# Kernel tuning notes

Hardware: AMD Instinct MI355X
Metric: run time of the kernel (lower is better)

The kernel has to match this reference:

```python
import jax, jax.numpy as jnp
import numpy as np

EPS = 1e-05


def layer_norm(x, a, b):
    m = jnp.mean(x, axis=-1, keepdims=True)
    v = jnp.var(x, axis=-1, keepdims=True)
    return a * (x - m) / jnp.sqrt(v + EPS) + b


def setup_inputs() -> dict:
    key = jax.random.key(0)
    ks = jax.random.split(key, 16)
    b, n, d, h = 1, 384, 128, 128
    s = 1.0 / np.sqrt(d)
    inp = {
        "x": jax.random.normal(ks[0], (b, n, n, d), dtype=jnp.float32),
        "norm_a": jnp.ones((d,), jnp.float32),
        "norm_b": jnp.zeros((d,), jnp.float32),
        "Wl": jax.random.normal(ks[1], (d, h), jnp.float32) * s,
        "bl": jnp.zeros((h,), jnp.float32),
        "Wr": jax.random.normal(ks[2], (d, h), jnp.float32) * s,
        "br": jnp.zeros((h,), jnp.float32),
        "Wlg": jax.random.normal(ks[3], (d, h), jnp.float32) * s,
        "blg": jnp.ones((h,), jnp.float32),
        "Wrg": jax.random.normal(ks[4], (d, h), jnp.float32) * s,
        "brg": jnp.ones((h,), jnp.float32),
        "Wog": jax.random.normal(ks[5], (d, h), jnp.float32) * s,
        "bog": jnp.ones((h,), jnp.float32),
        "on_a": jnp.ones((h,), jnp.float32),
        "on_b": jnp.zeros((h,), jnp.float32),
        "Wo": jax.random.normal(ks[6], (h, d), jnp.float32) * s,
        "bo": jnp.zeros((d,), jnp.float32),
    }
    return inp


def reference(x, norm_a, norm_b, Wl, bl, Wr, br, Wlg, blg, Wrg, brg, Wog, bog, on_a, on_b, Wo, bo):
    n = x.shape[1]
    xn = layer_norm(x, norm_a, norm_b)
    left = (xn @ Wl + bl) * jax.nn.sigmoid(xn @ Wlg + blg)
    right = (xn @ Wr + br) * jax.nn.sigmoid(xn @ Wrg + brg)
    out_gate = jax.nn.sigmoid(xn @ Wog + bog)
    # ingoing mix: out[b,i,j,d] = sum_k left[b,k,j,d] * right[b,k,i,d], in fp32
    out = jnp.einsum('bkjd,bkid->bijd', left.astype(jnp.float32), right.astype(jnp.float32)) / n
    out = out.astype(x.dtype)
    out = layer_norm(out, on_a, on_b) * out_gate
    return out @ Wo + bo
```

## Files before the change

### kernel.cpp

```cpp
#include <hip/hip_runtime.h>
#include <hip/hip_bf16.h>

#define NN 384
#define DD 128
#define MM (NN*NN)

typedef __attribute__((ext_vector_type(8))) short short8;
typedef __attribute__((ext_vector_type(4))) float f32x4;

__device__ __forceinline__ unsigned short f2bf(float f){
  unsigned u = __float_as_uint(f);
  u += 0x7fffu + ((u >> 16) & 1u);
  return (unsigned short)(u >> 16);
}
__device__ __forceinline__ float bf2f(unsigned short u){
  return __uint_as_float(((unsigned)u) << 16);
}
__device__ __forceinline__ float sigm(float x){
  return 1.0f / (1.0f + __expf(-x));
}
__device__ __forceinline__ unsigned cvtpk(float lo, float hi){
  unsigned r;
  asm("v_cvt_pk_bf16_f32 %0, %1, %2" : "=v"(r) : "v"(lo), "v"(hi));
  return r;
}
__device__ __forceinline__ f32x4 mfma16(short8 a, short8 b, f32x4 c){
  return __builtin_amdgcn_mfma_f32_16x16x32_bf16(a, b, c, 0, 0, 0);
}
__device__ __forceinline__ void gll16(const void* g, void* l){
  __builtin_amdgcn_global_load_lds(
      (const __attribute__((address_space(1))) unsigned int*)g,
      (__attribute__((address_space(3))) unsigned int*)l, 16, 0, 0);
}

__global__ void k_prep(const float* __restrict__ Wl, const float* __restrict__ Wlg,
                       const float* __restrict__ Wr, const float* __restrict__ Wrg,
                       const float* __restrict__ Wog, const float* __restrict__ Wo,
                       unsigned short* __restrict__ Wcat, unsigned short* __restrict__ Wot){
  int n = blockIdx.x;
  if(n < 640){
    const float* src; int col;
    if(n < 128){ src = Wl;  col = n; }
    else if(n < 256){ src = Wlg; col = n-128; }
    else if(n < 384){ src = Wr;  col = n-256; }
    else if(n < 512){ src = Wrg; col = n-384; }
    else            { src = Wog; col = n-512; }
    for(int k = threadIdx.x; k < 128; k += 64)
      Wcat[n*128 + k] = f2bf(src[k*128 + col]);
  } else {
    int c = n - 640;
    for(int k = threadIdx.x; k < 128; k += 64)
      Wot[c*128 + k] = f2bf(Wo[k*128 + c]);
  }
}

__global__ __launch_bounds__(256) void k_ln_x(const float* __restrict__ x,
    const float* __restrict__ na, const float* __restrict__ nb,
    unsigned short* __restrict__ xn){
  int wid = threadIdx.x >> 6, lane = threadIdx.x & 63;
  long r = (long)blockIdx.x*4 + wid;
  float2 v = *(const float2*)(x + r*DD + lane*2);
  float s  = v.x + v.y;
  float sq = v.x*v.x + v.y*v.y;
  #pragma unroll
  for(int m = 32; m >= 1; m >>= 1){ s += __shfl_xor(s, m); sq += __shfl_xor(sq, m); }
  float mean = s  * (1.0f/128.0f);
  float var  = sq * (1.0f/128.0f) - mean*mean;
  float rstd = rsqrtf(var + 1e-5f);
  float2 a = *(const float2*)(na + lane*2);
  float2 b = *(const float2*)(nb + lane*2);
  unsigned pk = (unsigned)f2bf(a.x*(v.x-mean)*rstd + b.x)
              | ((unsigned)f2bf(a.y*(v.y-mean)*rstd + b.y) << 16);
  *(unsigned*)(xn + r*DD + lane*2) = pk;
}

__global__ __launch_bounds__(512, 4) void k_proj(
    const unsigned short* __restrict__ xn, const unsigned short* __restrict__ Wcat,
    const float* __restrict__ bl, const float* __restrict__ blg,
    const float* __restrict__ br, const float* __restrict__ brg,
    const float* __restrict__ bog,
    unsigned short* __restrict__ Lt, unsigned short* __restrict__ Rt,
    unsigned short* __restrict__ gate){
  __shared__ char lds[65536];
  const int tid = threadIdx.x;
  const int wid = tid >> 6, lane = tid & 63;
  const int lrow = lane & 15, lgrp = lane >> 4;
  const int b = blockIdx.x;
  const int xcd = b & 7, slot = b >> 3;

  if(slot < 576){
    const int t = (slot >> 2)*8 + xcd;
    const int f = slot & 3;
    const int j0 = (t / 6)*2, k0 = (t % 6)*64;

    {
      int rsub = lane >> 4, c = lane & 15;
      #pragma unroll
      for(int p = 0; p < 4; ++p){
        int r0 = wid*16 + p*4;
        int r = r0 + rsub;
        long gr = (long)(k0 + (r & 63))*NN + (j0 + (r >> 6));
        gll16(xn + gr*DD + (c ^ (r & 7))*8, &lds[r0*256]);
      }
      #pragma unroll
      for(int p = 0; p < 4; ++p){
        int n0 = wid*16 + p*4;
        int nl = n0 + rsub;
        int ng = (nl >> 5)*128 + f*32 + (nl & 31);
        gll16(Wcat + ng*DD + (c ^ (nl & 7))*8, &lds[32768 + n0*256]);
      }
    }
    __syncthreads();

    const int ws = wid >> 2;
    const int wd = (wid >> 1) & 1;
    const int wr = wid & 1;
    f32x4 zero = {0.f,0.f,0.f,0.f};
    f32x4 acc[4][2];
    #pragma unroll
    for(int a1=0;a1<4;++a1){ acc[a1][0] = zero; acc[a1][1] = zero; }

    #pragma unroll 2
    for(int ks = 0; ks < 4; ++ks){
      int nlv = ws*64 + wd*16 + lrow;
      short8 bv = *(const short8*)(&lds[32768 + nlv*256 + (((ks*4+lgrp)*16) ^ ((nlv&7)<<4))]);
      int nlg = nlv + 32;
      short8 bg = *(const short8*)(&lds[32768 + nlg*256 + (((ks*4+lgrp)*16) ^ ((nlg&7)<<4))]);
      #pragma unroll
      for(int fr = 0; fr < 4; ++fr){
        int r = wr*64 + fr*16 + lrow;
        short8 af = *(const short8*)(&lds[r*256 + (((ks*4+lgrp)*16) ^ ((r&7)<<4))]);
        acc[fr][0] = mfma16(af, bv, acc[fr][0]);
        acc[fr][1] = mfma16(af, bg, acc[fr][1]);
      }
    }

    const int d = f*32 + wd*16 + lrow;
    const float b0v = (ws ? br  : bl )[d];
    const float b1v = (ws ? brg : blg)[d];
    const float sc = ws ? 1.0f : (1.0f/384.0f);
    unsigned short* dst = (ws ? Rt : Lt) + (long)d*MM + (long)(j0 + wr)*NN + k0;
    #pragma unroll
    for(int fr = 0; fr < 4; ++fr){
      float v0 = (acc[fr][0][0] + b0v)*sigm(acc[fr][1][0] + b1v)*sc;
      float v1 = (acc[fr][0][1] + b0v)*sigm(acc[fr][1][1] + b1v)*sc;
      float v2 = (acc[fr][0][2] + b0v)*sigm(acc[fr][1][2] + b1v)*sc;
      float v3 = (acc[fr][0][3] + b0v)*sigm(acc[fr][1][3] + b1v)*sc;
      uint2 pk; pk.x = cvtpk(v0, v1); pk.y = cvtpk(v2, v3);
      *(uint2*)(dst + fr*16 + lgrp*4) = pk;
    }
  } else {
    const int m = (slot - 576)*8 + xcd;
    {
      int rsub = lane >> 4, c = lane & 15;
      #pragma unroll
      for(int p = 0; p < 4; ++p){
        int r0 = wid*16 + p*4;
        int r = r0 + rsub;
        long gr = (long)m*128 + r;
        gll16(xn + gr*DD + (c ^ (r & 7))*8, &lds[r0*256]);
      }
      #pragma unroll
      for(int p = 0; p < 4; ++p){
        int n0 = wid*16 + p*4;
        int nl = n0 + rsub;
        gll16(Wcat + (512 + nl)*DD + (c ^ (nl & 7))*8, &lds[32768 + n0*256]);
      }
    }
    __syncthreads();

    const int wm = wid >> 2;
    const int wc = wid & 3;
    f32x4 zero = {0.f,0.f,0.f,0.f};
    f32x4 acc[2][4];
    #pragma unroll
    for(int a1=0;a1<2;++a1)
      #pragma unroll
      for(int a2=0;a2<4;++a2) acc[a1][a2] = zero;

    #pragma unroll 2
    for(int ks = 0; ks < 4; ++ks){
      short8 af[2];
      #pragma unroll
      for(int cf = 0; cf < 2; ++cf){
        int nl = wc*32 + cf*16 + lrow;
        af[cf] = *(const short8*)(&lds[32768 + nl*256 + (((ks*4+lgrp)*16) ^ ((nl&7)<<4))]);
      }
      #pragma unroll
      for(int mf = 0; mf < 4; ++mf){
        int r = wm*64 + mf*16 + lrow;
        short8 bfr = *(const short8*)(&lds[r*256 + (((ks*4+lgrp)*16) ^ ((r&7)<<4))]);
        acc[0][mf] = mfma16(af[0], bfr, acc[0][mf]);
        acc[1][mf] = mfma16(af[1], bfr, acc[1][mf]);
      }
    }

    #pragma unroll
    for(int cf = 0; cf < 2; ++cf){
      int c = wc*32 + cf*16 + lgrp*4;
      float4 bo4 = *(const float4*)(bog + c);
      #pragma unroll
      for(int mf = 0; mf < 4; ++mf){
        int rr = wm*64 + mf*16 + lrow;
        float v0 = sigm(acc[cf][mf][0] + bo4.x);
        float v1 = sigm(acc[cf][mf][1] + bo4.y);
        float v2 = sigm(acc[cf][mf][2] + bo4.z);
        float v3 = sigm(acc[cf][mf][3] + bo4.w);
        uint2 pk; pk.x = cvtpk(v0, v1); pk.y = cvtpk(v2, v3);
        *(uint2*)(gate + ((long)m*128 + rr)*DD + c) = pk;
      }
    }
  }
}

__global__ __launch_bounds__(256) void k_einsum(
    const unsigned short* __restrict__ Rt, const unsigned short* __restrict__ Lt,
    unsigned short* __restrict__ mid){
  __shared__ char lds[65536];
  const int b = blockIdx.x;
  const int xcd = b & 7, slot = b >> 3;
  const int d = (slot/9)*8 + xcd;
  const int t = slot % 9;
  const int it = t/3, jt = t%3;
  const int i0 = it*128, j0 = jt*128;
  const unsigned short* Abase = Lt + (long)d*MM;
  const unsigned short* Bbase = Rt + (long)d*MM;
  const int wid = threadIdx.x >> 6, lane = threadIdx.x & 63;
  const int wr = wid >> 1, wc = wid & 1;
  const int lrow = lane & 15, lgrp = lane >> 4;

  auto stage = [&](int buf, int kt){
    int k = kt*64;
    int c = lane & 7;
    #pragma unroll
    for(int t8 = 0; t8 < 8; ++t8){
      int rr = wid*64 + t8*8 + (lane >> 3);
      int r = rr & 127;
      const unsigned short* src = (rr < 128) ? (Abase + (long)(j0+r)*NN + k)
                                             : (Bbase + (long)(i0+r)*NN + k);
      gll16(src + (c ^ (r & 7))*8, &lds[buf*32768 + (wid*64 + t8*8)*128]);
    }
  };

  f32x4 zero = {0.f,0.f,0.f,0.f};
  f32x4 acc[4][4];
  #pragma unroll
  for(int a1 = 0; a1 < 4; ++a1)
    #pragma unroll
    for(int a2 = 0; a2 < 4; ++a2) acc[a1][a2] = zero;

  stage(0, 0);
  __syncthreads();
  for(int kt = 0; kt < 6; ++kt){
    int cur = kt & 1;
    if(kt < 5) stage(cur ^ 1, kt + 1);
    const int base = cur*32768;
    #pragma unroll
    for(int ks = 0; ks < 2; ++ks){
      short8 af[4], bf[4];
      #pragma unroll
      for(int f = 0; f < 4; ++f){
        int rj = wr*64 + f*16 + lrow;
        af[f] = *(const short8*)(&lds[base + rj*128 + (((ks*4+lgrp)*16) ^ ((rj & 7) << 4))]);
        int ri = wc*64 + f*16 + lrow;
        bf[f] = *(const short8*)(&lds[base + 16384 + ri*128 + (((ks*4+lgrp)*16) ^ ((ri & 7) << 4))]);
      }
      #pragma unroll
      for(int fj = 0; fj < 4; ++fj)
        #pragma unroll
        for(int fi = 0; fi < 4; ++fi)
          acc[fj][fi] = mfma16(af[fj], bf[fi], acc[fj][fi]);
    }
    __syncthreads();
  }

  #pragma unroll
  for(int fj = 0; fj < 4; ++fj){
    int j = j0 + wr*64 + fj*16 + lgrp*4;
    #pragma unroll
    for(int fi = 0; fi < 4; ++fi){
      int i = i0 + wc*64 + fi*16 + lrow;
      uint2 pk;
      pk.x = cvtpk(acc[fj][fi][0], acc[fj][fi][1]);
      pk.y = cvtpk(acc[fj][fi][2], acc[fj][fi][3]);
      *(uint2*)(mid + (long)d*MM + (long)i*NN + j) = pk;
    }
  }
}

__global__ __launch_bounds__(256) void k_final(
    const unsigned short* __restrict__ mid, const unsigned short* __restrict__ gate,
    const float* __restrict__ ona, const float* __restrict__ onb,
    const unsigned short* __restrict__ Wot, const float* __restrict__ bo,
    float* __restrict__ out){
  __shared__ float midt[64][129];
  __shared__ char vlds[16384];
  const int tid = threadIdx.x;
  const int i = blockIdx.y;
  const int j0 = blockIdx.x*64;

  {
    int jp = tid & 15, dr = tid >> 4;
    #pragma unroll
    for(int pass = 0; pass < 8; ++pass){
      int dd = pass*16 + dr;
      uint2 v = *(const uint2*)(mid + (long)dd*MM + (long)i*NN + j0 + jp*4);
      midt[jp*4+0][dd] = bf2f((unsigned short)(v.x & 0xffffu));
      midt[jp*4+1][dd] = bf2f((unsigned short)(v.x >> 16));
      midt[jp*4+2][dd] = bf2f((unsigned short)(v.y & 0xffffu));
      midt[jp*4+3][dd] = bf2f((unsigned short)(v.y >> 16));
    }
  }
  __syncthreads();

  {
    int j = tid >> 2, s = tid & 3;
    float sum = 0.f, sq = 0.f;
    #pragma unroll
    for(int o = 0; o < 32; ++o){ float v = midt[j][s*32 + o]; sum += v; sq += v*v; }
    #pragma unroll
    for(int m = 1; m < 4; m <<= 1){ sum += __shfl_xor(sum, m); sq += __shfl_xor(sq, m); }
    float mean = sum*(1.f/128.f);
    float var  = sq *(1.f/128.f) - mean*mean;
    float rstd = rsqrtf(var + 1e-5f);
    long gr = ((long)i*NN + j0 + j)*DD;
    #pragma unroll
    for(int o = 0; o < 32; o += 4){
      int dd = s*32 + o;
      uint2 gv = *(const uint2*)(gate + gr + dd);
      float g0 = bf2f((unsigned short)(gv.x & 0xffffu));
      float g1 = bf2f((unsigned short)(gv.x >> 16));
      float g2 = bf2f((unsigned short)(gv.y & 0xffffu));
      float g3 = bf2f((unsigned short)(gv.y >> 16));
      float v0 = (ona[dd]  *(midt[j][dd]  -mean)*rstd + onb[dd]  )*g0;
      float v1 = (ona[dd+1]*(midt[j][dd+1]-mean)*rstd + onb[dd+1])*g1;
      float v2 = (ona[dd+2]*(midt[j][dd+2]-mean)*rstd + onb[dd+2])*g2;
      float v3 = (ona[dd+3]*(midt[j][dd+3]-mean)*rstd + onb[dd+3])*g3;
      unsigned pk01 = cvtpk(v0, v1);
      unsigned pk23 = cvtpk(v2, v3);
      *(unsigned*)(&vlds[j*256 + ((dd*2)     ^ ((j & 7) << 4))]) = pk01;
      *(unsigned*)(&vlds[j*256 + ((dd*2 + 4) ^ ((j & 7) << 4))]) = pk23;
    }
  }
  __syncthreads();

  const int wid = tid >> 6, lane = tid & 63;
  const int lrow = lane & 15, lgrp = lane >> 4;
  f32x4 zero = {0.f,0.f,0.f,0.f};
  f32x4 acc[8];
  #pragma unroll
  for(int fc = 0; fc < 8; ++fc) acc[fc] = zero;
  #pragma unroll 1
  for(int ks = 0; ks < 4; ++ks){
    int row = wid*16 + lrow;
    short8 a = *(const short8*)(&vlds[row*256 + (((ks*4+lgrp)*16) ^ ((row & 7) << 4))]);
    #pragma unroll
    for(int fc = 0; fc < 8; ++fc){
      int n = fc*16 + lrow;
      short8 bfr = *(const short8*)(Wot + n*128 + ks*32 + lgrp*8);
      acc[fc] = mfma16(a, bfr, acc[fc]);
    }
  }
  #pragma unroll
  for(int fc = 0; fc < 8; ++fc){
    int c = fc*16 + lrow;
    float bb = bo[c];
    #pragma unroll
    for(int q = 0; q < 4; ++q){
      int jl = wid*16 + lgrp*4 + q;
      out[((long)i*NN + j0 + jl)*DD + c] = acc[fc][q] + bb;
    }
  }
}

extern "C" void kernel_launch(void* const* d_in, const int* in_sizes, int n_in,
                              void* d_out, int out_size, void* d_ws, size_t ws_size,
                              hipStream_t stream){
  const float* x   = (const float*)d_in[0];
  const float* na  = (const float*)d_in[1];
  const float* nb  = (const float*)d_in[2];
  const float* Wl  = (const float*)d_in[3];
  const float* bl  = (const float*)d_in[4];
  const float* Wr  = (const float*)d_in[5];
  const float* br  = (const float*)d_in[6];
  const float* Wlg = (const float*)d_in[7];
  const float* blg = (const float*)d_in[8];
  const float* Wrg = (const float*)d_in[9];
  const float* brg = (const float*)d_in[10];
  const float* Wog = (const float*)d_in[11];
  const float* bog = (const float*)d_in[12];
  const float* ona = (const float*)d_in[13];
  const float* onb = (const float*)d_in[14];
  const float* Wo  = (const float*)d_in[15];
  const float* bo  = (const float*)d_in[16];
  float* out = (float*)d_out;

  char* ws = (char*)d_ws;
  const size_t SZ = (size_t)MM*DD*2;
  unsigned short* xn   = (unsigned short*)(ws);
  unsigned short* Lt   = (unsigned short*)(ws + SZ);
  unsigned short* Rt   = (unsigned short*)(ws + 2*SZ);
  unsigned short* gate = (unsigned short*)(ws + 3*SZ);
  unsigned short* Wcat = (unsigned short*)(ws + 4*SZ);
  unsigned short* Wot  = (unsigned short*)(ws + 4*SZ + (size_t)640*128*2);
  unsigned short* mid  = xn;

  k_prep  <<<768, 64, 0, stream>>>(Wl, Wlg, Wr, Wrg, Wog, Wo, Wcat, Wot);
  k_ln_x  <<<MM/4, 256, 0, stream>>>(x, na, nb, xn);
  k_proj  <<<5760, 512, 0, stream>>>(xn, Wcat, bl, blg, br, brg, bog, Lt, Rt, gate);
  k_einsum<<<1152, 256, 0, stream>>>(Rt, Lt, mid);
  k_final <<<dim3(6, 384), 256, 0, stream>>>(mid, gate, ona, onb, Wot, bo, out);
}
```

Measured before the change: 200.3 us.

## Move output-gate projection into final kernel and make proj kernel persistent with double buffering

New measurement: 197.2 us. Within noise of the previous version (-1.6%).

```diff
diff --git a/kernel.cpp b/kernel.cpp
--- a/kernel.cpp
+++ b/kernel.cpp
@@ -74,72 +74,70 @@
   *(unsigned*)(xn + r*DD + lane*2) = pk;
 }
 
-__global__ __launch_bounds__(512, 4) void k_proj(
+__global__ __launch_bounds__(256, 4) void k_proj(
     const unsigned short* __restrict__ xn, const unsigned short* __restrict__ Wcat,
     const float* __restrict__ bl, const float* __restrict__ blg,
     const float* __restrict__ br, const float* __restrict__ brg,
-    const float* __restrict__ bog,
-    unsigned short* __restrict__ Lt, unsigned short* __restrict__ Rt,
-    unsigned short* __restrict__ gate){
-  __shared__ char lds[65536];
+    unsigned short* __restrict__ Lt, unsigned short* __restrict__ Rt){
+  __shared__ char lds[2][16384];
   const int tid = threadIdx.x;
   const int wid = tid >> 6, lane = tid & 63;
   const int lrow = lane & 15, lgrp = lane >> 4;
   const int b = blockIdx.x;
-  const int xcd = b & 7, slot = b >> 3;
-
-  if(slot < 576){
-    const int t = (slot >> 2)*8 + xcd;
-    const int f = slot & 3;
-    const int j0 = (t / 6)*2, k0 = (t % 6)*64;
-
-    {
-      int rsub = lane >> 4, c = lane & 15;
-      #pragma unroll
-      for(int p = 0; p < 4; ++p){
-        int r0 = wid*16 + p*4;
-        int r = r0 + rsub;
-        long gr = (long)(k0 + (r & 63))*NN + (j0 + (r >> 6));
-        gll16(xn + gr*DD + (c ^ (r & 7))*8, &lds[r0*256]);
-      }
-      #pragma unroll
-      for(int p = 0; p < 4; ++p){
-        int n0 = wid*16 + p*4;
-        int nl = n0 + rsub;
-        int ng = (nl >> 5)*128 + f*32 + (nl & 31);
-        gll16(Wcat + ng*DD + (c ^ (nl & 7))*8, &lds[32768 + n0*256]);
-      }
-    }
-    __syncthreads();
-
-    const int ws = wid >> 2;
-    const int wd = (wid >> 1) & 1;
-    const int wr = wid & 1;
+  const int f = b / 288;
+  const int w = b % 288;
+
+  const int ws = wid >> 1;
+  const int wd = wid & 1;
+  const int d  = f*32 + wd*16 + lrow;
+
+  short8 bv[4], bg[4];
+  #pragma unroll
+  for(int ks = 0; ks < 4; ++ks){
+    bv[ks] = *(const short8*)(Wcat + (ws*256 + d)*DD + ks*32 + lgrp*8);
+    bg[ks] = *(const short8*)(Wcat + (ws*256 + 128 + d)*DD + ks*32 + lgrp*8);
+  }
+  const float b0v = (ws ? br  : bl )[d];
+  const float b1v = (ws ? brg : blg)[d];
+  const float sc  = ws ? 1.0f : (1.0f/384.0f);
+  unsigned short* const base = (ws ? Rt : Lt) + (long)d*MM;
+
+  auto stage = [&](int buf, int v){
+    int j = v/6, kb = v%6;
+    int rsub = lane >> 4, c = lane & 15;
+    #pragma unroll
+    for(int p = 0; p < 4; ++p){
+      int r0 = p*16 + wid*4;
+      int r = r0 + rsub;
+      gll16(xn + ((long)(kb*64 + r)*NN + j)*DD + (c ^ (r & 7))*8, &lds[buf][r0*256]);
+    }
+  };
+
+  stage(0, w*8);
+  __syncthreads();
+  int cur = 0;
+  for(int i = 0; i < 8; ++i){
+    int v = w*8 + i;
+    if(i < 7) stage(cur^1, v+1);
+
     f32x4 zero = {0.f,0.f,0.f,0.f};
     f32x4 acc[4][2];
     #pragma unroll
     for(int a1=0;a1<4;++a1){ acc[a1][0] = zero; acc[a1][1] = zero; }
 
-    #pragma unroll 2
+    #pragma unroll
     for(int ks = 0; ks < 4; ++ks){
-      int nlv = ws*64 + wd*16 + lrow;
-      short8 bv = *(const short8*)(&lds[32768 + nlv*256 + (((ks*4+lgrp)*16) ^ ((nlv&7)<<4))]);
-      int nlg = nlv + 32;
-      short8 bg = *(const short8*)(&lds[32768 + nlg*256 + (((ks*4+lgrp)*16) ^ ((nlg&7)<<4))]);
       #pragma unroll
       for(int fr = 0; fr < 4; ++fr){
-        int r = wr*64 + fr*16 + lrow;
-        short8 af = *(const short8*)(&lds[r*256 + (((ks*4+lgrp)*16) ^ ((r&7)<<4))]);
-        acc[fr][0] = mfma16(af, bv, acc[fr][0]);
-        acc[fr][1] = mfma16(af, bg, acc[fr][1]);
-      }
-    }
-
-    const int d = f*32 + wd*16 + lrow;
-    const float b0v = (ws ? br  : bl )[d];
-    const float b1v = (ws ? brg : blg)[d];
-    const float sc = ws ? 1.0f : (1.0f/384.0f);
-    unsigned short* dst = (ws ? Rt : Lt) + (long)d*MM + (long)(j0 + wr)*NN + k0;
+        int r = fr*16 + lrow;
+        short8 af = *(const short8*)(&lds[cur][r*256 + (((ks*4+lgrp)*16) ^ ((r&7)<<4))]);
+        acc[fr][0] = mfma16(af, bv[ks], acc[fr][0]);
+        acc[fr][1] = mfma16(af, bg[ks], acc[fr][1]);
+      }
+    }
+
+    int j = v/6, kb = v%6;
+    unsigned short* dst = base + (long)j*NN + kb*64;
     #pragma unroll
     for(int fr = 0; fr < 4; ++fr){
       float v0 = (acc[fr][0][0] + b0v)*sigm(acc[fr][1][0] + b1v)*sc;
@@ -149,67 +147,8 @@
       uint2 pk; pk.x = cvtpk(v0, v1); pk.y = cvtpk(v2, v3);
       *(uint2*)(dst + fr*16 + lgrp*4) = pk;
     }
-  } else {
-    const int m = (slot - 576)*8 + xcd;
-    {
-      int rsub = lane >> 4, c = lane & 15;
-      #pragma unroll
-      for(int p = 0; p < 4; ++p){
-        int r0 = wid*16 + p*4;
-        int r = r0 + rsub;
-        long gr = (long)m*128 + r;
-        gll16(xn + gr*DD + (c ^ (r & 7))*8, &lds[r0*256]);
-      }
-      #pragma unroll
-      for(int p = 0; p < 4; ++p){
-        int n0 = wid*16 + p*4;
-        int nl = n0 + rsub;
-        gll16(Wcat + (512 + nl)*DD + (c ^ (nl & 7))*8, &lds[32768 + n0*256]);
-      }
-    }
     __syncthreads();
-
-    const int wm = wid >> 2;
-    const int wc = wid & 3;
-    f32x4 zero = {0.f,0.f,0.f,0.f};
-    f32x4 acc[2][4];
-    #pragma unroll
-    for(int a1=0;a1<2;++a1)
-      #pragma unroll
-      for(int a2=0;a2<4;++a2) acc[a1][a2] = zero;
-
-    #pragma unroll 2
-    for(int ks = 0; ks < 4; ++ks){
-      short8 af[2];
-      #pragma unroll
-      for(int cf = 0; cf < 2; ++cf){
-        int nl = wc*32 + cf*16 + lrow;
-        af[cf] = *(const short8*)(&lds[32768 + nl*256 + (((ks*4+lgrp)*16) ^ ((nl&7)<<4))]);
-      }
-      #pragma unroll
-      for(int mf = 0; mf < 4; ++mf){
-        int r = wm*64 + mf*16 + lrow;
-        short8 bfr = *(const short8*)(&lds[r*256 + (((ks*4+lgrp)*16) ^ ((r&7)<<4))]);
-        acc[0][mf] = mfma16(af[0], bfr, acc[0][mf]);
-        acc[1][mf] = mfma16(af[1], bfr, acc[1][mf]);
-      }
-    }
-
-    #pragma unroll
-    for(int cf = 0; cf < 2; ++cf){
-      int c = wc*32 + cf*16 + lgrp*4;
-      float4 bo4 = *(const float4*)(bog + c);
-      #pragma unroll
-      for(int mf = 0; mf < 4; ++mf){
-        int rr = wm*64 + mf*16 + lrow;
-        float v0 = sigm(acc[cf][mf][0] + bo4.x);
-        float v1 = sigm(acc[cf][mf][1] + bo4.y);
-        float v2 = sigm(acc[cf][mf][2] + bo4.z);
-        float v3 = sigm(acc[cf][mf][3] + bo4.w);
-        uint2 pk; pk.x = cvtpk(v0, v1); pk.y = cvtpk(v2, v3);
-        *(uint2*)(gate + ((long)m*128 + rr)*DD + c) = pk;
-      }
-    }
+    cur ^= 1;
   }
 }
 
@@ -289,15 +228,37 @@
 }
 
 __global__ __launch_bounds__(256) void k_final(
-    const unsigned short* __restrict__ mid, const unsigned short* __restrict__ gate,
+    const unsigned short* __restrict__ mid, const unsigned short* __restrict__ xn,
+    const unsigned short* __restrict__ Wcat,
+    const float* __restrict__ bog,
     const float* __restrict__ ona, const float* __restrict__ onb,
     const unsigned short* __restrict__ Wot, const float* __restrict__ bo,
     float* __restrict__ out){
-  __shared__ float midt[64][129];
-  __shared__ char vlds[16384];
+  __shared__ unsigned short midt[64][144];
+  __shared__ char slds[16384];
+  __shared__ char glds[16384];
   const int tid = threadIdx.x;
+  const int wid = tid >> 6, lane = tid & 63;
+  const int lrow = lane & 15, lgrp = lane >> 4;
   const int i = blockIdx.y;
   const int j0 = blockIdx.x*64;
+
+  {
+    int rsub = lane >> 4, c = lane & 15;
+    #pragma unroll
+    for(int p = 0; p < 4; ++p){
+      int r0 = p*16 + wid*4;
+      int r = r0 + rsub;
+      gll16(xn + ((long)i*NN + j0 + r)*DD + (c ^ (r & 7))*8, &slds[r0*256]);
+    }
+  }
+  const int wc = wid;
+  short8 ag[2][4];
+  #pragma unroll
+  for(int cf = 0; cf < 2; ++cf)
+    #pragma unroll
+    for(int ks = 0; ks < 4; ++ks)
+      ag[cf][ks] = *(const short8*)(Wcat + (512 + wc*32 + cf*16 + lrow)*DD + ks*32 + lgrp*8);
 
   {
     int jp = tid & 15, dr = tid >> 4;
@@ -305,70 +266,114 @@
     for(int pass = 0; pass < 8; ++pass){
       int dd = pass*16 + dr;
       uint2 v = *(const uint2*)(mid + (long)dd*MM + (long)i*NN + j0 + jp*4);
-      midt[jp*4+0][dd] = bf2f((unsigned short)(v.x & 0xffffu));
-      midt[jp*4+1][dd] = bf2f((unsigned short)(v.x >> 16));
-      midt[jp*4+2][dd] = bf2f((unsigned short)(v.y & 0xffffu));
-      midt[jp*4+3][dd] = bf2f((unsigned short)(v.y >> 16));
+      midt[jp*4+0][dd] = (unsigned short)(v.x & 0xffffu);
+      midt[jp*4+1][dd] = (unsigned short)(v.x >> 16);
+      midt[jp*4+2][dd] = (unsigned short)(v.y & 0xffffu);
+      midt[jp*4+3][dd] = (unsigned short)(v.y >> 16);
+    }
+  }
+  __syncthreads();
+
+  {
+    f32x4 zero = {0.f,0.f,0.f,0.f};
+    f32x4 accg[2][4];
+    #pragma unroll
+    for(int a1=0;a1<2;++a1)
+      #pragma unroll
+      for(int a2=0;a2<4;++a2) accg[a1][a2] = zero;
+    #pragma unroll
+    for(int ks = 0; ks < 4; ++ks){
+      short8 bx[4];
+      #pragma unroll
+      for(int mf = 0; mf < 4; ++mf){
+        int r = mf*16 + lrow;
+        bx[mf] = *(const short8*)(&slds[r*256 + (((ks*4+lgrp)*16) ^ ((r&7)<<4))]);
+      }
+      #pragma unroll
+      for(int cf = 0; cf < 2; ++cf)
+        #pragma unroll
+        for(int mf = 0; mf < 4; ++mf)
+          accg[cf][mf] = mfma16(ag[cf][ks], bx[mf], accg[cf][mf]);
+    }
+    #pragma unroll
+    for(int cf = 0; cf < 2; ++cf){
+      int c0 = wc*32 + cf*16 + lgrp*4;
+      float4 b4 = *(const float4*)(bog + c0);
+      #pragma unroll
+      for(int mf = 0; mf < 4; ++mf){
+        int rr = mf*16 + lrow;
+        uint2 pk;
+        pk.x = cvtpk(sigm(accg[cf][mf][0] + b4.x), sigm(accg[cf][mf][1] + b4.y));
+        pk.y = cvtpk(sigm(accg[cf][mf][2] + b4.z), sigm(accg[cf][mf][3] + b4.w));
+        *(uint2*)(&glds[rr*256 + ((c0*2) ^ ((rr&7)<<4))]) = pk;
+      }
     }
   }
   __syncthreads();
 
   {
     int j = tid >> 2, s = tid & 3;
+    float vals[32];
     float sum = 0.f, sq = 0.f;
     #pragma unroll
-    for(int o = 0; o < 32; ++o){ float v = midt[j][s*32 + o]; sum += v; sq += v*v; }
+    for(int o8 = 0; o8 < 4; ++o8){
+      short8 h = *(const short8*)(&midt[j][s*32 + o8*8]);
+      #pragma unroll
+      for(int q = 0; q < 8; ++q){
+        float vq = bf2f((unsigned short)h[q]);
+        vals[o8*8+q] = vq; sum += vq; sq += vq*vq;
+      }
+    }
     #pragma unroll
     for(int m = 1; m < 4; m <<= 1){ sum += __shfl_xor(sum, m); sq += __shfl_xor(sq, m); }
     float mean = sum*(1.f/128.f);
     float var  = sq *(1.f/128.f) - mean*mean;
     float rstd = rsqrtf(var + 1e-5f);
-    long gr = ((long)i*NN + j0 + j)*DD;
     #pragma unroll
     for(int o = 0; o < 32; o += 4){
       int dd = s*32 + o;
-      uint2 gv = *(const uint2*)(gate + gr + dd);
+      uint2 gv = *(const uint2*)(&glds[j*256 + ((dd*2) ^ ((j&7)<<4))]);
       float g0 = bf2f((unsigned short)(gv.x & 0xffffu));
       float g1 = bf2f((unsigned short)(gv.x >> 16));
       float g2 = bf2f((unsigned short)(gv.y & 0xffffu));
       float g3 = bf2f((unsigned short)(gv.y >> 16));
-      float v0 = (ona[dd]  *(midt[j][dd]  -mean)*rstd + onb[dd]  )*g0;
-      float v1 = (ona[dd+1]*(midt[j][dd+1]-mean)*rstd + onb[dd+1])*g1;
-      float v2 = (ona[dd+2]*(midt[j][dd+2]-mean)*rstd + onb[dd+2])*g2;
-      float v3 = (ona[dd+3]*(midt[j][dd+3]-mean)*rstd + onb[dd+3])*g3;
-      unsigned pk01 = cvtpk(v0, v1);
-      unsigned pk23 = cvtpk(v2, v3);
-      *(unsigned*)(&vlds[j*256 + ((dd*2)     ^ ((j & 7) << 4))]) = pk01;
-      *(unsigned*)(&vlds[j*256 + ((dd*2 + 4) ^ ((j & 7) << 4))]) = pk23;
+      float4 a4 = *(const float4*)(ona + dd);
+      float4 b4 = *(const float4*)(onb + dd);
+      float v0 = (a4.x*(vals[o]  -mean)*rstd + b4.x)*g0;
+      float v1 = (a4.y*(vals[o+1]-mean)*rstd + b4.y)*g1;
+      float v2 = (a4.z*(vals[o+2]-mean)*rstd + b4.z)*g2;
+      float v3 = (a4.w*(vals[o+3]-mean)*rstd + b4.w)*g3;
+      uint2 pk; pk.x = cvtpk(v0, v1); pk.y = cvtpk(v2, v3);
+      *(uint2*)(&slds[j*256 + ((dd*2) ^ ((j&7)<<4))]) = pk;
     }
   }
   __syncthreads();
 
-  const int wid = tid >> 6, lane = tid & 63;
-  const int lrow = lane & 15, lgrp = lane >> 4;
-  f32x4 zero = {0.f,0.f,0.f,0.f};
-  f32x4 acc[8];
-  #pragma unroll
-  for(int fc = 0; fc < 8; ++fc) acc[fc] = zero;
-  #pragma unroll 1
-  for(int ks = 0; ks < 4; ++ks){
-    int row = wid*16 + lrow;
-    short8 a = *(const short8*)(&vlds[row*256 + (((ks*4+lgrp)*16) ^ ((row & 7) << 4))]);
+  {
+    f32x4 zero = {0.f,0.f,0.f,0.f};
+    f32x4 acc[8];
+    #pragma unroll
+    for(int fc = 0; fc < 8; ++fc) acc[fc] = zero;
+    #pragma unroll 1
+    for(int ks = 0; ks < 4; ++ks){
+      int row = wid*16 + lrow;
+      short8 a = *(const short8*)(&slds[row*256 + (((ks*4+lgrp)*16) ^ ((row & 7) << 4))]);
+      #pragma unroll
+      for(int fc = 0; fc < 8; ++fc){
+        int n = fc*16 + lrow;
+        short8 bfr = *(const short8*)(Wot + n*DD + ks*32 + lgrp*8);
+        acc[fc] = mfma16(a, bfr, acc[fc]);
+      }
+    }
     #pragma unroll
     for(int fc = 0; fc < 8; ++fc){
-      int n = fc*16 + lrow;
-      short8 bfr = *(const short8*)(Wot + n*128 + ks*32 + lgrp*8);
-      acc[fc] = mfma16(a, bfr, acc[fc]);
-    }
-  }
-  #pragma unroll
-  for(int fc = 0; fc < 8; ++fc){
-    int c = fc*16 + lrow;
-    float bb = bo[c];
-    #pragma unroll
-    for(int q = 0; q < 4; ++q){
-      int jl = wid*16 + lgrp*4 + q;
-      out[((long)i*NN + j0 + jl)*DD + c] = acc[fc][q] + bb;
+      int c = fc*16 + lrow;
+      float bb = bo[c];
+      #pragma unroll
+      for(int q = 0; q < 4; ++q){
+        int jl = wid*16 + lgrp*4 + q;
+        out[((long)i*NN + j0 + jl)*DD + c] = acc[fc][q] + bb;
+      }
     }
   }
 }
@@ -400,14 +405,13 @@
   unsigned short* xn   = (unsigned short*)(ws);
   unsigned short* Lt   = (unsigned short*)(ws + SZ);
   unsigned short* Rt   = (unsigned short*)(ws + 2*SZ);
-  unsigned short* gate = (unsigned short*)(ws + 3*SZ);
+  unsigned short* mid  = (unsigned short*)(ws + 3*SZ);
   unsigned short* Wcat = (unsigned short*)(ws + 4*SZ);
   unsigned short* Wot  = (unsigned short*)(ws + 4*SZ + (size_t)640*128*2);
-  unsigned short* mid  = xn;
 
   k_prep  <<<768, 64, 0, stream>>>(Wl, Wlg, Wr, Wrg, Wog, Wo, Wcat, Wot);
   k_ln_x  <<<MM/4, 256, 0, stream>>>(x, na, nb, xn);
-  k_proj  <<<5760, 512, 0, stream>>>(xn, Wcat, bl, blg, br, brg, bog, Lt, Rt, gate);
+  k_proj  <<<1152, 256, 0, stream>>>(xn, Wcat, bl, blg, br, brg, Lt, Rt);
   k_einsum<<<1152, 256, 0, stream>>>(Rt, Lt, mid);
-  k_final <<<dim3(6, 384), 256, 0, stream>>>(mid, gate, ona, onb, Wot, bo, out);
-}
+  k_final <<<dim3(6, 384), 256, 0, stream>>>(mid, xn, Wcat, bog, ona, onb, Wot, bo, out);
+}
```
